# Kernel tuning notes

Hardware: AMD Instinct MI355X
Metric: run time of the kernel (lower is better)

Reference implementation:

```python
import jax, jax.numpy as jnp
import numpy as np

N_NODES = 50000
N_EDGES = 1600000


def gcn_conv(h, W, b, src, dst, ew, n_nodes):
    """PyG GCNConv: linear -> add self-loops (weight 1) -> sym-norm scatter-add -> bias."""
    h = h @ W                                   # [N, out]
    loop = jnp.arange(n_nodes, dtype=src.dtype)
    s = jnp.concatenate([src, loop])            # [E+N]
    d = jnp.concatenate([dst, loop])
    w = jnp.concatenate([ew, jnp.ones((n_nodes,), dtype=h.dtype)])
    deg = jax.ops.segment_sum(w, d, num_segments=n_nodes)          # in-degree (weighted)
    dinv = jnp.where(deg > 0, jax.lax.rsqrt(deg), 0.0)
    coef = dinv[s] * w * dinv[d]                # D^-1/2 A D^-1/2 per-edge coefficient
    msg = h[s] * coef[:, None]                  # gather + scale  [E+N, out]
    out = jax.ops.segment_sum(msg, d, num_segments=n_nodes)        # scatter-add
    return out + b


def setup_inputs() -> dict:
    key = jax.random.key(0)
    ks = jax.random.split(key, 6)
    x = jax.random.normal(ks[0], (N_NODES, 256), dtype=jnp.float32)
    edge_index = jax.random.randint(ks[1], (2, N_EDGES), 0, N_NODES, dtype=jnp.int64)
    edge_weight = jax.random.uniform(ks[2], (N_EDGES,), dtype=jnp.float32)
    W1 = jax.random.normal(ks[3], (256, 128), dtype=jnp.float32) * (1.0 / np.sqrt(256))
    b1 = jnp.zeros((128,), dtype=jnp.float32)
    W2 = jax.random.normal(ks[4], (128, 64), dtype=jnp.float32) * (1.0 / np.sqrt(128))
    b2 = jnp.zeros((64,), dtype=jnp.float32)
    return {"x": x, "edge_index": edge_index, "edge_weight": edge_weight,
            "W1": W1, "b1": b1, "W2": W2, "b2": b2}


def reference(x, edge_index, edge_weight, W1, b1, W2, b2):
    src, dst = edge_index[0], edge_index[1]
    n = x.shape[0]
    h = gcn_conv(x, W1, b1, src, dst, edge_weight, n)
    h = jax.nn.relu(h)
    # dropout is identity in eval mode
    out = gcn_conv(h, W2, b2, src, dst, edge_weight, n)
    return out
```

## Files before the change

kernel.cpp:

```cpp
#include <hip/hip_runtime.h>

#define NN 50000
#define NE 1600000
#define NB 391
#define NBLK 128
#define NSEG 50048

typedef short bf16x8 __attribute__((ext_vector_type(8)));
typedef float f32x4 __attribute__((ext_vector_type(4)));

static __device__ __forceinline__ unsigned f2bf(float f) {
    union { float f; unsigned u; } v; v.f = f;
    return (v.u + 0x7FFF + ((v.u >> 16) & 1)) >> 16;
}

__global__ __launch_bounds__(256) void p1_hist(const int* __restrict__ dst,
        int* __restrict__ cntB) {
    __shared__ int h[NB];
    for (int i = threadIdx.x; i < NB; i += 256) h[i] = 0;
    __syncthreads();
    int base = blockIdx.x * 12500;
    for (int k = threadIdx.x; k < 12500; k += 256)
        atomicAdd(&h[dst[base + k] >> 7], 1);
    __syncthreads();
    for (int i = threadIdx.x; i < NB; i += 256)
        cntB[i * NBLK + blockIdx.x] = h[i];
}

__global__ __launch_bounds__(256) void scan1_kernel(const int* __restrict__ in,
        int* __restrict__ csum, int* __restrict__ bsum) {
    __shared__ int sd[256];
    int t = threadIdx.x;
    int idx = blockIdx.x * 256 + t;
    int v = (idx < NSEG) ? in[idx] : 0;
    sd[t] = v;
    __syncthreads();
    for (int off = 1; off < 256; off <<= 1) {
        int x = (t >= off) ? sd[t - off] : 0;
        __syncthreads();
        sd[t] += x;
        __syncthreads();
    }
    if (idx < NSEG) csum[idx + 1] = sd[t];
    if (t == 255) bsum[blockIdx.x] = sd[255];
}

__global__ __launch_bounds__(256) void scan2_kernel(int* __restrict__ bsum,
        int* __restrict__ csum) {
    __shared__ int sd[256];
    int t = threadIdx.x;
    int v = (t < 196) ? bsum[t] : 0;
    sd[t] = v;
    __syncthreads();
    for (int off = 1; off < 256; off <<= 1) {
        int x = (t >= off) ? sd[t - off] : 0;
        __syncthreads();
        sd[t] += x;
        __syncthreads();
    }
    if (t < 196) bsum[t] = sd[t] - v;
    if (t == 0) csum[0] = 0;
}

__global__ __launch_bounds__(256) void scan3_kernel(int* __restrict__ csum,
        const int* __restrict__ bsum) {
    int idx = blockIdx.x * 256 + threadIdx.x;
    if (idx < NSEG) csum[idx + 1] += bsum[blockIdx.x];
}

__global__ __launch_bounds__(256) void p3_scatter(const int* __restrict__ src,
        const int* __restrict__ dst, const float* __restrict__ ew,
        const int* __restrict__ csum, int2* __restrict__ ebuf) {
    __shared__ int curs[NB];
    for (int i = threadIdx.x; i < NB; i += 256)
        curs[i] = csum[i * NBLK + blockIdx.x];
    __syncthreads();
    int base = blockIdx.x * 12500;
    for (int k = threadIdx.x; k < 12500; k += 256) {
        int d = dst[base + k];
        int s = src[base + k];
        float w = ew[base + k];
        int pos = atomicAdd(&curs[d >> 7], 1);
        ebuf[pos] = make_int2(s | ((d & 127) << 16), __float_as_int(w));
    }
}

__global__ __launch_bounds__(256) void p4_build(const int2* __restrict__ ebuf,
        const int* __restrict__ csum, int2* __restrict__ edata,
        float* __restrict__ dinv, int* __restrict__ rowptr) {
    __shared__ int cnt[128], loff[128], cur[128], sd[128];
    __shared__ float deg[128];
    int bk = blockIdx.x;
    int t = threadIdx.x;
    int ebase = csum[bk * 128];
    int ecnt = csum[(bk + 1) * 128] - ebase;
    if (t < 128) { cnt[t] = 0; cur[t] = 0; deg[t] = 0.0f; }
    __syncthreads();
    for (int i = t; i < ecnt; i += 256) {
        int2 e = ebuf[ebase + i];
        int dl = (e.x >> 16) & 127;
        atomicAdd(&cnt[dl], 1);
        atomicAdd(&deg[dl], __int_as_float(e.y));
    }
    __syncthreads();
    if (t < 128) sd[t] = cnt[t];
    __syncthreads();
    for (int off = 1; off < 128; off <<= 1) {
        int v = 0;
        if (t < 128 && t >= off) v = sd[t - off];
        __syncthreads();
        if (t < 128) sd[t] += v;
        __syncthreads();
    }
    if (t < 128) loff[t] = sd[t] - cnt[t];
    __syncthreads();
    int node = bk * 128 + t;
    if (t < 128 && node < NN) {
        dinv[node] = rsqrtf(deg[t] + 1.0f);
        rowptr[node] = ebase + loff[t];
    }
    if (bk == NB - 1 && t == 0) rowptr[NN] = NE;
    for (int i = t; i < ecnt; i += 256) {
        int2 e = ebuf[ebase + i];
        int dl = (e.x >> 16) & 127;
        int slot = loff[dl] + atomicAdd(&cur[dl], 1);
        edata[ebase + slot] = make_int2(e.x & 0xFFFF, e.y);
    }
}

__global__ __launch_bounds__(256) void wt_kernel(const float* __restrict__ W1,
        const float* __restrict__ W2, ushort* __restrict__ Wt1,
        ushort* __restrict__ Wt2) {
    int idx = blockIdx.x * 256 + threadIdx.x;
    if (idx < 32768) {
        int k = idx >> 7, n = idx & 127;
        Wt1[n * 256 + k] = (ushort)f2bf(W1[idx]);
    } else if (idx < 40960) {
        int i = idx - 32768;
        int k = i >> 6, n = i & 63;
        Wt2[n * 128 + k] = (ushort)f2bf(W2[i]);
    }
}

__global__ __launch_bounds__(256) void gemm1_kernel(const float* __restrict__ A,
        const ushort* __restrict__ Bt, ushort* __restrict__ C,
        const float* __restrict__ dinv, int M) {
    const int K = 256, N = 128;
    __shared__ __align__(16) ushort As[64][72];
    __shared__ __align__(16) ushort Bs[128][72];
    int tid = threadIdx.x;
    int bm = blockIdx.x * 64;
    int w = tid >> 6, lane = tid & 63;
    int m = lane & 15, quad = lane >> 4;
    f32x4 acc[8] = {};
    int ra = tid >> 2, ksa = (tid & 3) * 16;
    int rb = tid >> 1, ksb = (tid & 1) * 32;
    int grow = bm + ra; if (grow >= M) grow = M - 1;
    const float* ap = A + (size_t)grow * K + ksa;
    const ushort* bp = Bt + (size_t)rb * K + ksb;
    for (int k0 = 0; k0 < K; k0 += 64) {
        float4 f0 = *(const float4*)(ap + k0);
        float4 f1 = *(const float4*)(ap + k0 + 4);
        float4 f2 = *(const float4*)(ap + k0 + 8);
        float4 f3 = *(const float4*)(ap + k0 + 12);
        uint4 bv0 = *(const uint4*)(bp + k0);
        uint4 bv1 = *(const uint4*)(bp + k0 + 8);
        uint4 bv2 = *(const uint4*)(bp + k0 + 16);
        uint4 bv3 = *(const uint4*)(bp + k0 + 24);
        uint4 pa, pb;
        pa.x = f2bf(f0.x) | (f2bf(f0.y) << 16);
        pa.y = f2bf(f0.z) | (f2bf(f0.w) << 16);
        pa.z = f2bf(f1.x) | (f2bf(f1.y) << 16);
        pa.w = f2bf(f1.z) | (f2bf(f1.w) << 16);
        pb.x = f2bf(f2.x) | (f2bf(f2.y) << 16);
        pb.y = f2bf(f2.z) | (f2bf(f2.w) << 16);
        pb.z = f2bf(f3.x) | (f2bf(f3.y) << 16);
        pb.w = f2bf(f3.z) | (f2bf(f3.w) << 16);
        __syncthreads();
        *(uint4*)&As[ra][ksa] = pa;
        *(uint4*)&As[ra][ksa + 8] = pb;
        *(uint4*)&Bs[rb][ksb] = bv0;
        *(uint4*)&Bs[rb][ksb + 8] = bv1;
        *(uint4*)&Bs[rb][ksb + 16] = bv2;
        *(uint4*)&Bs[rb][ksb + 24] = bv3;
        __syncthreads();
        #pragma unroll
        for (int ks = 0; ks < 2; ++ks) {
            bf16x8 a = *(const bf16x8*)&As[w * 16 + m][ks * 32 + quad * 8];
            #pragma unroll
            for (int t = 0; t < 8; ++t) {
                bf16x8 b = *(const bf16x8*)&Bs[t * 16 + m][ks * 32 + quad * 8];
                acc[t] = __builtin_amdgcn_mfma_f32_16x16x32_bf16(a, b, acc[t], 0, 0, 0);
            }
        }
    }
    int rbase = bm + w * 16 + quad * 4;
    float dv[4];
    #pragma unroll
    for (int rg = 0; rg < 4; ++rg)
        dv[rg] = (rbase + rg < M) ? dinv[rbase + rg] : 0.0f;
    #pragma unroll
    for (int t = 0; t < 8; ++t) {
        int col = t * 16 + m;
        #pragma unroll
        for (int rg = 0; rg < 4; ++rg) {
            int row = rbase + rg;
            if (row < M)
                C[(size_t)row * N + col] = (ushort)f2bf(dv[rg] * acc[t][rg]);
        }
    }
}

__global__ __launch_bounds__(256) void gemm2_kernel(const ushort* __restrict__ A,
        const ushort* __restrict__ Bt, ushort* __restrict__ C,
        const float* __restrict__ dinv, int M) {
    const int K = 128, N = 64;
    __shared__ __align__(16) ushort As[64][72];
    __shared__ __align__(16) ushort Bs[64][72];
    int tid = threadIdx.x;
    int bm = blockIdx.x * 64;
    int w = tid >> 6, lane = tid & 63;
    int m = lane & 15, quad = lane >> 4;
    f32x4 acc[4] = {};
    int r = tid >> 2, ks0 = (tid & 3) * 16;
    int grow = bm + r; if (grow >= M) grow = M - 1;
    const ushort* ap = A + (size_t)grow * K + ks0;
    const ushort* bp = Bt + (size_t)r * K + ks0;
    for (int k0 = 0; k0 < K; k0 += 64) {
        uint4 av0 = *(const uint4*)(ap + k0);
        uint4 av1 = *(const uint4*)(ap + k0 + 8);
        uint4 bv0 = *(const uint4*)(bp + k0);
        uint4 bv1 = *(const uint4*)(bp + k0 + 8);
        __syncthreads();
        *(uint4*)&As[r][ks0] = av0;
        *(uint4*)&As[r][ks0 + 8] = av1;
        *(uint4*)&Bs[r][ks0] = bv0;
        *(uint4*)&Bs[r][ks0 + 8] = bv1;
        __syncthreads();
        #pragma unroll
        for (int ks = 0; ks < 2; ++ks) {
            bf16x8 a = *(const bf16x8*)&As[w * 16 + m][ks * 32 + quad * 8];
            #pragma unroll
            for (int t = 0; t < 4; ++t) {
                bf16x8 b = *(const bf16x8*)&Bs[t * 16 + m][ks * 32 + quad * 8];
                acc[t] = __builtin_amdgcn_mfma_f32_16x16x32_bf16(a, b, acc[t], 0, 0, 0);
            }
        }
    }
    int rbase = bm + w * 16 + quad * 4;
    float dv[4];
    #pragma unroll
    for (int rg = 0; rg < 4; ++rg)
        dv[rg] = (rbase + rg < M) ? dinv[rbase + rg] : 0.0f;
    #pragma unroll
    for (int t = 0; t < 4; ++t) {
        int col = t * 16 + m;
        #pragma unroll
        for (int rg = 0; rg < 4; ++rg) {
            int row = rbase + rg;
            if (row < M)
                C[(size_t)row * N + col] = (ushort)f2bf(dv[rg] * acc[t][rg]);
        }
    }
}

template<int F, int LPN, int RELU, int OUTBF>
__global__ __launch_bounds__(256) void agg_csr_kernel(
        const int* __restrict__ rowptr, const int2* __restrict__ edata,
        const ushort* __restrict__ H, const float* __restrict__ dinv,
        const float* __restrict__ bias, void* __restrict__ outv) {
    constexpr int NPB = 256 / LPN;
    int node = blockIdx.x * NPB + threadIdx.x / LPN;
    if (node >= NN) return;
    int glane = threadIdx.x & (LPN - 1);
    int gb = (threadIdx.x & 63) & ~(LPN - 1);
    int beg = rowptr[node], end = rowptr[node + 1];
    float acc[8] = {};
    const ushort* Hl = H + (size_t)glane * 8;
    for (int chunk = beg; chunk < end; chunk += LPN) {
        int nch = end - chunk; if (nch > LPN) nch = LPN;
        int edx = 0, edy = 0;
        if (glane < nch) {
            int2 e = edata[chunk + glane];
            edx = e.x; edy = e.y;
        }
        int j = 0;
        for (; j + 2 <= nch; j += 2) {
            int s0 = __shfl(edx, gb + j);
            int s1 = __shfl(edx, gb + j + 1);
            float c0 = __int_as_float(__shfl(edy, gb + j));
            float c1 = __int_as_float(__shfl(edy, gb + j + 1));
            uint4 h0 = *(const uint4*)(Hl + (size_t)s0 * F);
            uint4 h1 = *(const uint4*)(Hl + (size_t)s1 * F);
            const unsigned* u0 = (const unsigned*)&h0;
            const unsigned* u1 = (const unsigned*)&h1;
            #pragma unroll
            for (int q = 0; q < 4; ++q) {
                acc[2*q]   += __uint_as_float(u0[q] << 16) * c0;
                acc[2*q+1] += __uint_as_float(u0[q] & 0xFFFF0000u) * c0;
            }
            #pragma unroll
            for (int q = 0; q < 4; ++q) {
                acc[2*q]   += __uint_as_float(u1[q] << 16) * c1;
                acc[2*q+1] += __uint_as_float(u1[q] & 0xFFFF0000u) * c1;
            }
        }
        if (j < nch) {
            int s0 = __shfl(edx, gb + j);
            float c0 = __int_as_float(__shfl(edy, gb + j));
            uint4 h0 = *(const uint4*)(Hl + (size_t)s0 * F);
            const unsigned* u0 = (const unsigned*)&h0;
            #pragma unroll
            for (int q = 0; q < 4; ++q) {
                acc[2*q]   += __uint_as_float(u0[q] << 16) * c0;
                acc[2*q+1] += __uint_as_float(u0[q] & 0xFFFF0000u) * c0;
            }
        }
    }
    float di = dinv[node];
    uint4 hn = *(const uint4*)(Hl + (size_t)node * F);
    const unsigned* un = (const unsigned*)&hn;
    float4 bv0 = *(const float4*)(bias + glane * 8);
    float4 bv1 = *(const float4*)(bias + glane * 8 + 4);
    float v[8];
    #pragma unroll
    for (int q = 0; q < 4; ++q) {
        v[2*q]   = di * (acc[2*q]   + __uint_as_float(un[q] << 16));
        v[2*q+1] = di * (acc[2*q+1] + __uint_as_float(un[q] & 0xFFFF0000u));
    }
    v[0] += bv0.x; v[1] += bv0.y; v[2] += bv0.z; v[3] += bv0.w;
    v[4] += bv1.x; v[5] += bv1.y; v[6] += bv1.z; v[7] += bv1.w;
    if (RELU) {
        #pragma unroll
        for (int k = 0; k < 8; ++k) v[k] = fmaxf(v[k], 0.0f);
    }
    if (OUTBF) {
        uint4 o;
        o.x = f2bf(v[0]) | (f2bf(v[1]) << 16);
        o.y = f2bf(v[2]) | (f2bf(v[3]) << 16);
        o.z = f2bf(v[4]) | (f2bf(v[5]) << 16);
        o.w = f2bf(v[6]) | (f2bf(v[7]) << 16);
        *(uint4*)((ushort*)outv + (size_t)node * F + glane * 8) = o;
    } else {
        float* o = (float*)outv + (size_t)node * F + glane * 8;
        *(float4*)(o)     = make_float4(v[0], v[1], v[2], v[3]);
        *(float4*)(o + 4) = make_float4(v[4], v[5], v[6], v[7]);
    }
}

extern "C" void kernel_launch(void* const* d_in, const int* in_sizes, int n_in,
                              void* d_out, int out_size, void* d_ws, size_t ws_size,
                              hipStream_t stream) {
    const float* x  = (const float*)d_in[0];
    const int*   ei = (const int*)d_in[1];
    const float* ew = (const float*)d_in[2];
    const float* W1 = (const float*)d_in[3];
    const float* b1 = (const float*)d_in[4];
    const float* W2 = (const float*)d_in[5];
    const float* b2 = (const float*)d_in[6];
    const int* src = ei;
    const int* dst = ei + NE;
    float* out = (float*)d_out;

    float* ws     = (float*)d_ws;
    float* dinv   = ws;
    int*   rowptr = (int*)(ws + 50048);
    int*   csum   = (int*)(ws + 100112);
    int*   bsum   = (int*)(ws + 150176);
    int*   cntB   = (int*)(ws + 150528);
    ushort* Wt1   = (ushort*)(ws + 200576);
    ushort* Wt2   = Wt1 + 32768;
    int2*  edata  = (int2*)(ws + 221056);
    ushort* H1    = (ushort*)(ws + 3421056);
    ushort* A1    = (ushort*)(ws + 6621056);
    int2*  ebuf   = (int2*)A1;

    p1_hist<<<NBLK, 256, 0, stream>>>(dst, cntB);
    scan1_kernel<<<196, 256, 0, stream>>>(cntB, csum, bsum);
    scan2_kernel<<<1, 256, 0, stream>>>(bsum, csum);
    scan3_kernel<<<196, 256, 0, stream>>>(csum, bsum);
    wt_kernel<<<160, 256, 0, stream>>>(W1, W2, Wt1, Wt2);
    p3_scatter<<<NBLK, 256, 0, stream>>>(src, dst, ew, csum, ebuf);
    p4_build<<<NB, 256, 0, stream>>>(ebuf, csum, edata, dinv, rowptr);

    gemm1_kernel<<<782, 256, 0, stream>>>(x, Wt1, H1, dinv, NN);
    agg_csr_kernel<128, 16, 1, 1><<<3125, 256, 0, stream>>>(rowptr, edata, H1, dinv, b1, A1);

    gemm2_kernel<<<782, 256, 0, stream>>>(A1, Wt2, H1, dinv, NN);
    agg_csr_kernel<64, 8, 0, 0><<<1563, 256, 0, stream>>>(rowptr, edata, H1, dinv, b2, out);
}
```

Before: 266.1 us.

## Fuse layer-1 aggregation with layer-2 GEMM and merge scan into one kernel

The layer-1 CSR aggregation now writes its 16 node rows (bias, relu, bf16) to shared memory and immediately multiplies them by W2 with MFMA, writing the dinv-scaled H2. This removes the A1 round trip through global memory and the separate gemm2 launch. The three-kernel prefix scan is also replaced by a single-block kernel that processes 4096 elements per pass, saving two launches but serialising the scan on one workgroup. Each aggregation block now reads W2 directly from global memory instead of staging it in LDS.

Measured after the change: 311.6 us. 17.1% more time.

```diff
diff --git a/kernel.cpp b/kernel.cpp
--- a/kernel.cpp
+++ b/kernel.cpp
@@ -27,45 +27,42 @@
         cntB[i * NBLK + blockIdx.x] = h[i];
 }
 
-__global__ __launch_bounds__(256) void scan1_kernel(const int* __restrict__ in,
-        int* __restrict__ csum, int* __restrict__ bsum) {
-    __shared__ int sd[256];
-    int t = threadIdx.x;
-    int idx = blockIdx.x * 256 + t;
-    int v = (idx < NSEG) ? in[idx] : 0;
-    sd[t] = v;
-    __syncthreads();
-    for (int off = 1; off < 256; off <<= 1) {
-        int x = (t >= off) ? sd[t - off] : 0;
-        __syncthreads();
-        sd[t] += x;
-        __syncthreads();
-    }
-    if (idx < NSEG) csum[idx + 1] = sd[t];
-    if (t == 255) bsum[blockIdx.x] = sd[255];
-}
-
-__global__ __launch_bounds__(256) void scan2_kernel(int* __restrict__ bsum,
+__global__ __launch_bounds__(256) void scan_all_kernel(const int* __restrict__ in,
         int* __restrict__ csum) {
     __shared__ int sd[256];
+    __shared__ int sbase;
     int t = threadIdx.x;
-    int v = (t < 196) ? bsum[t] : 0;
-    sd[t] = v;
-    __syncthreads();
-    for (int off = 1; off < 256; off <<= 1) {
-        int x = (t >= off) ? sd[t - off] : 0;
-        __syncthreads();
-        sd[t] += x;
-        __syncthreads();
-    }
-    if (t < 196) bsum[t] = sd[t] - v;
-    if (t == 0) csum[0] = 0;
-}
-
-__global__ __launch_bounds__(256) void scan3_kernel(int* __restrict__ csum,
-        const int* __restrict__ bsum) {
-    int idx = blockIdx.x * 256 + threadIdx.x;
-    if (idx < NSEG) csum[idx + 1] += bsum[blockIdx.x];
+    if (t == 0) { sbase = 0; csum[0] = 0; }
+    __syncthreads();
+    for (int c0 = 0; c0 < NSEG; c0 += 4096) {
+        int vals[16];
+        int sum = 0;
+        int base_idx = c0 + t * 16;
+        #pragma unroll
+        for (int k = 0; k < 16; ++k) {
+            int idx = base_idx + k;
+            vals[k] = (idx < NSEG) ? in[idx] : 0;
+            sum += vals[k];
+        }
+        sd[t] = sum;
+        __syncthreads();
+        for (int off = 1; off < 256; off <<= 1) {
+            int v = (t >= off) ? sd[t - off] : 0;
+            __syncthreads();
+            sd[t] += v;
+            __syncthreads();
+        }
+        int running = sbase + sd[t] - sum;
+        #pragma unroll
+        for (int k = 0; k < 16; ++k) {
+            int idx = base_idx + k;
+            running += vals[k];
+            if (idx < NSEG) csum[idx + 1] = running;
+        }
+        __syncthreads();
+        if (t == 0) sbase += sd[255];
+        __syncthreads();
+    }
 }
 
 __global__ __launch_bounds__(256) void p3_scatter(const int* __restrict__ src,
@@ -211,56 +208,97 @@
     }
 }
 
-__global__ __launch_bounds__(256) void gemm2_kernel(const ushort* __restrict__ A,
-        const ushort* __restrict__ Bt, ushort* __restrict__ C,
-        const float* __restrict__ dinv, int M) {
-    const int K = 128, N = 64;
-    __shared__ __align__(16) ushort As[64][72];
-    __shared__ __align__(16) ushort Bs[64][72];
+__global__ __launch_bounds__(256) void agg1_fused_kernel(
+        const int* __restrict__ rowptr, const int2* __restrict__ edata,
+        const ushort* __restrict__ H, const float* __restrict__ dinv,
+        const float* __restrict__ bias, const ushort* __restrict__ Wt2,
+        ushort* __restrict__ H2) {
+    __shared__ __align__(16) ushort Ats[16][136];
     int tid = threadIdx.x;
-    int bm = blockIdx.x * 64;
+    int nl = tid >> 4;
+    int node = blockIdx.x * 16 + nl;
+    int glane = tid & 15;
+    int gb = (tid & 63) & ~15;
+    int beg = rowptr[node], end = rowptr[node + 1];
+    float acc[8] = {};
+    const ushort* Hl = H + (size_t)glane * 8;
+    for (int chunk = beg; chunk < end; chunk += 16) {
+        int nch = end - chunk; if (nch > 16) nch = 16;
+        int edx = 0, edy = 0;
+        if (glane < nch) {
+            int2 e = edata[chunk + glane];
+            edx = e.x; edy = e.y;
+        }
+        int j = 0;
+        for (; j + 2 <= nch; j += 2) {
+            int s0 = __shfl(edx, gb + j);
+            int s1 = __shfl(edx, gb + j + 1);
+            float c0 = __int_as_float(__shfl(edy, gb + j));
+            float c1 = __int_as_float(__shfl(edy, gb + j + 1));
+            uint4 h0 = *(const uint4*)(Hl + (size_t)s0 * 128);
+            uint4 h1 = *(const uint4*)(Hl + (size_t)s1 * 128);
+            const unsigned* u0 = (const unsigned*)&h0;
+            const unsigned* u1 = (const unsigned*)&h1;
+            #pragma unroll
+            for (int q = 0; q < 4; ++q) {
+                acc[2*q]   += __uint_as_float(u0[q] << 16) * c0;
+                acc[2*q+1] += __uint_as_float(u0[q] & 0xFFFF0000u) * c0;
+            }
+            #pragma unroll
+            for (int q = 0; q < 4; ++q) {
+                acc[2*q]   += __uint_as_float(u1[q] << 16) * c1;
+                acc[2*q+1] += __uint_as_float(u1[q] & 0xFFFF0000u) * c1;
+            }
+        }
+        if (j < nch) {
+            int s0 = __shfl(edx, gb + j);
+            float c0 = __int_as_float(__shfl(edy, gb + j));
+            uint4 h0 = *(const uint4*)(Hl + (size_t)s0 * 128);
+            const unsigned* u0 = (const unsigned*)&h0;
+            #pragma unroll
+            for (int q = 0; q < 4; ++q) {
+                acc[2*q]   += __uint_as_float(u0[q] << 16) * c0;
+                acc[2*q+1] += __uint_as_float(u0[q] & 0xFFFF0000u) * c0;
+            }
+        }
+    }
+    float di = dinv[node];
+    uint4 hn = *(const uint4*)(Hl + (size_t)node * 128);
+    const unsigned* un = (const unsigned*)&hn;
+    float4 bv0 = *(const float4*)(bias + glane * 8);
+    float4 bv1 = *(const float4*)(bias + glane * 8 + 4);
+    float v[8];
+    #pragma unroll
+    for (int q = 0; q < 4; ++q) {
+        v[2*q]   = di * (acc[2*q]   + __uint_as_float(un[q] << 16));
+        v[2*q+1] = di * (acc[2*q+1] + __uint_as_float(un[q] & 0xFFFF0000u));
+    }
+    v[0] += bv0.x; v[1] += bv0.y; v[2] += bv0.z; v[3] += bv0.w;
+    v[4] += bv1.x; v[5] += bv1.y; v[6] += bv1.z; v[7] += bv1.w;
+    #pragma unroll
+    for (int k = 0; k < 8; ++k) v[k] = fmaxf(v[k], 0.0f);
+    uint4 o;
+    o.x = f2bf(v[0]) | (f2bf(v[1]) << 16);
+    o.y = f2bf(v[2]) | (f2bf(v[3]) << 16);
+    o.z = f2bf(v[4]) | (f2bf(v[5]) << 16);
+    o.w = f2bf(v[6]) | (f2bf(v[7]) << 16);
+    *(uint4*)&Ats[nl][glane * 8] = o;
+    __syncthreads();
     int w = tid >> 6, lane = tid & 63;
     int m = lane & 15, quad = lane >> 4;
-    f32x4 acc[4] = {};
-    int r = tid >> 2, ks0 = (tid & 3) * 16;
-    int grow = bm + r; if (grow >= M) grow = M - 1;
-    const ushort* ap = A + (size_t)grow * K + ks0;
-    const ushort* bp = Bt + (size_t)r * K + ks0;
-    for (int k0 = 0; k0 < K; k0 += 64) {
-        uint4 av0 = *(const uint4*)(ap + k0);
-        uint4 av1 = *(const uint4*)(ap + k0 + 8);
-        uint4 bv0 = *(const uint4*)(bp + k0);
-        uint4 bv1 = *(const uint4*)(bp + k0 + 8);
-        __syncthreads();
-        *(uint4*)&As[r][ks0] = av0;
-        *(uint4*)&As[r][ks0 + 8] = av1;
-        *(uint4*)&Bs[r][ks0] = bv0;
-        *(uint4*)&Bs[r][ks0 + 8] = bv1;
-        __syncthreads();
-        #pragma unroll
-        for (int ks = 0; ks < 2; ++ks) {
-            bf16x8 a = *(const bf16x8*)&As[w * 16 + m][ks * 32 + quad * 8];
-            #pragma unroll
-            for (int t = 0; t < 4; ++t) {
-                bf16x8 b = *(const bf16x8*)&Bs[t * 16 + m][ks * 32 + quad * 8];
-                acc[t] = __builtin_amdgcn_mfma_f32_16x16x32_bf16(a, b, acc[t], 0, 0, 0);
-            }
-        }
-    }
-    int rbase = bm + w * 16 + quad * 4;
-    float dv[4];
-    #pragma unroll
-    for (int rg = 0; rg < 4; ++rg)
-        dv[rg] = (rbase + rg < M) ? dinv[rbase + rg] : 0.0f;
-    #pragma unroll
-    for (int t = 0; t < 4; ++t) {
-        int col = t * 16 + m;
-        #pragma unroll
-        for (int rg = 0; rg < 4; ++rg) {
-            int row = rbase + rg;
-            if (row < M)
-                C[(size_t)row * N + col] = (ushort)f2bf(dv[rg] * acc[t][rg]);
-        }
+    const ushort* bp = Wt2 + (size_t)(w * 16 + m) * 128 + quad * 8;
+    f32x4 c2 = {};
+    #pragma unroll
+    for (int kc = 0; kc < 4; ++kc) {
+        bf16x8 a = *(const bf16x8*)&Ats[m][kc * 32 + quad * 8];
+        bf16x8 b = *(const bf16x8*)(bp + kc * 32);
+        c2 = __builtin_amdgcn_mfma_f32_16x16x32_bf16(a, b, c2, 0, 0, 0);
+    }
+    int rbase = blockIdx.x * 16 + quad * 4;
+    #pragma unroll
+    for (int rg = 0; rg < 4; ++rg) {
+        float dvr = dinv[rbase + rg];
+        H2[(size_t)(rbase + rg) * 64 + w * 16 + m] = (ushort)f2bf(dvr * c2[rg]);
     }
 }
 
@@ -366,26 +404,21 @@
     float* dinv   = ws;
     int*   rowptr = (int*)(ws + 50048);
     int*   csum   = (int*)(ws + 100112);
-    int*   bsum   = (int*)(ws + 150176);
     int*   cntB   = (int*)(ws + 150528);
     ushort* Wt1   = (ushort*)(ws + 200576);
     ushort* Wt2   = Wt1 + 32768;
     int2*  edata  = (int2*)(ws + 221056);
     ushort* H1    = (ushort*)(ws + 3421056);
-    ushort* A1    = (ushort*)(ws + 6621056);
-    int2*  ebuf   = (int2*)A1;
+    ushort* H2    = (ushort*)(ws + 6621056);
+    int2*  ebuf   = (int2*)H2;
 
     p1_hist<<<NBLK, 256, 0, stream>>>(dst, cntB);
-    scan1_kernel<<<196, 256, 0, stream>>>(cntB, csum, bsum);
-    scan2_kernel<<<1, 256, 0, stream>>>(bsum, csum);
-    scan3_kernel<<<196, 256, 0, stream>>>(csum, bsum);
+    scan_all_kernel<<<1, 256, 0, stream>>>(cntB, csum);
     wt_kernel<<<160, 256, 0, stream>>>(W1, W2, Wt1, Wt2);
     p3_scatter<<<NBLK, 256, 0, stream>>>(src, dst, ew, csum, ebuf);
     p4_build<<<NB, 256, 0, stream>>>(ebuf, csum, edata, dinv, rowptr);
 
     gemm1_kernel<<<782, 256, 0, stream>>>(x, Wt1, H1, dinv, NN);
-    agg_csr_kernel<128, 16, 1, 1><<<3125, 256, 0, stream>>>(rowptr, edata, H1, dinv, b1, A1);
-
-    gemm2_kernel<<<782, 256, 0, stream>>>(A1, Wt2, H1, dinv, NN);
-    agg_csr_kernel<64, 8, 0, 0><<<1563, 256, 0, stream>>>(rowptr, edata, H1, dinv, b2, out);
-}
+    agg1_fused_kernel<<<3125, 256, 0, stream>>>(rowptr, edata, H1, dinv, b1, Wt2, H2);
+    agg_csr_kernel<64, 8, 0, 0><<<1563, 256, 0, stream>>>(rowptr, edata, H2, dinv, b2, out);
+}
```
